# Kernel tuning notes

Hardware: AMD Instinct MI355X
Metric: run time of the kernel (lower is better)

The kernel has to match this reference:

```python
import jax, jax.numpy as jnp
import numpy as np

B, N, C = 128, 1024, 1
N_TIMES = 2
NUM_SUBSTEPS = 279  # trunc(dt_Output/dt_sub)+1 for default params


def setup_inputs() -> dict:
    key = jax.random.key(0)
    # small amplitude: d_to_u multiplies spectrum by k (up to N/2), keep CFL stable
    x = jax.random.normal(key, (B, N, C), dtype=jnp.float32) * 1e-3
    return {
        "x": x,
        "nu_para": jnp.float32(-3.0),
        "dt_Output_para": jnp.float32(-3.0),
        "cRatio_para": jnp.float32(0.1),
        "nTimes": N_TIMES,
        "num_substeps": NUM_SUBSTEPS,
    }


def _forward(x, nu_para, dt_Output_para, cRatio_para, nTimes, num_substeps):
    n = x.shape[1]
    L = 2.0 * np.pi
    k = (2.0 * np.pi / L) * jnp.arange(n // 2 + 1, dtype=jnp.float32)  # [n//2+1]
    ik = 1j * k

    # reparameterized physical params (sigmoid squashing, as in the torch module)
    nu = jax.nn.sigmoid(nu_para) * (0.5 - 0.01) + 0.01
    dt_out = jax.nn.sigmoid(dt_Output_para) * (0.1 - 0.001) + 0.001
    cR = jax.nn.sigmoid(cRatio_para) * (2.0 - 0.5) + 0.5

    d = jnp.transpose(x, (0, 2, 1))  # [B, C, N]
    # d_to_u: u = irfft(1j * rfft(d) * k)
    u = jnp.fft.irfft(1j * jnp.fft.rfft(d) * k, n=n)

    dt = dt_out / num_substeps
    # q = 1 - dt*cR*(k + nu*(1j*k)^2) ; (1j*k)^2 = -k^2 so q is real-valued
    q = 1.0 - dt * cR * (k - nu * k * k)

    def substep(u, _):
        uhat = jnp.fft.rfft(u)
        u2hat = jnp.fft.rfft(0.5 * u * u)
        u_new = jnp.fft.irfft((uhat - dt * ik * u2hat) / q, n=n)
        return u_new, None

    def outer(u, _):
        u, _ = jax.lax.scan(substep, u, None, length=num_substeps)
        return u, u

    _, usol = jax.lax.scan(outer, u, None, length=nTimes)  # [T, B, C, N]
    T = usol.shape[0]
    # torch.cat(usol, dim=1): [B, T*C, N] with time-major ordering
    usol = jnp.moveaxis(usol, 0, 1).reshape(usol.shape[1], T * usol.shape[2], n)

    # u_to_d: d_hat = -1j*rfft(u); d_hat[...,1:] /= k[1:]; d_hat[...,0] = 0
    d_hat = -1j * jnp.fft.rfft(usol)
    safe_k = jnp.where(k > 0, k, 1.0)
    d_hat = jnp.where(k > 0, d_hat / safe_k, jnp.zeros((), dtype=d_hat.dtype))
    dsol = jnp.fft.irfft(d_hat, n=n)  # [B, T*C, N]

    return jnp.transpose(dsol, (0, 2, 1))  # [B, N, T*C]


def reference(x, nu_para, dt_Output_para, cRatio_para, nTimes, num_substeps):
    return _forward(x, nu_para, dt_Output_para, cRatio_para, nTimes, num_substeps)
```

## Files before the change

### kernel.cpp

```cpp
#include <hip/hip_runtime.h>
#include <math.h>

#define NFFT 1024
#define BLK  512

template <int CTRL>
__device__ __forceinline__ float dppf(float v) {
    return __int_as_float(__builtin_amdgcn_update_dpp(
        0, __float_as_int(v), CTRL, 0xF, 0xF, true));
}
__device__ __forceinline__ float qx1(float v) { return dppf<0xB1>(v); }
__device__ __forceinline__ float qx2(float v) { return dppf<0x4E>(v); }
__device__ __forceinline__ float xr4(float v) { return dppf<0x1B>(dppf<0x141>(v)); }
__device__ __forceinline__ float xr8(float v) { return dppf<0x128>(v); }

__device__ __forceinline__ void pswap16(float v, float& lo, float& hi) {
    auto r = __builtin_amdgcn_permlane16_swap(__float_as_int(v), __float_as_int(v),
                                              false, false);
    lo = __int_as_float(r[0]);
    hi = __int_as_float(r[1]);
}
__device__ __forceinline__ void pswap32(float v, float& lo, float& hi) {
    auto r = __builtin_amdgcn_permlane32_swap(__float_as_int(v), __float_as_int(v),
                                              false, false);
    lo = __int_as_float(r[0]);
    hi = __int_as_float(r[1]);
}

#define DECL_G(G) float2 G##0, G##1, G##2, G##3, G##4, G##5, G##6, G##7,       \
                         G##8, G##9, G##10, G##11, G##12, G##13, G##14, G##15

#define GROW(Gd, d)                                                             \
    {   float sx = 0.0f, sy = 0.0f;                                             \
        _Pragma("unroll")                                                       \
        for (int ka = 0; ka < 16; ++ka) {                                       \
            const float ang = (float)((d) * ka) * 0.125f;                       \
            sx = fmaf(mv[ka], cospif(ang), sx);                                 \
            sy = fmaf(mv[ka], -sinpif(ang), sy);                                \
        }                                                                       \
        Gd = make_float2(sx, sy); }

#define BUILD_G(G)                                                              \
    GROW(G##0, 0)  GROW(G##1, 1)  GROW(G##2, 2)   GROW(G##3, 3)                 \
    GROW(G##4, 4)  GROW(G##5, 5)  GROW(G##6, 6)   GROW(G##7, 7)                 \
    GROW(G##8, 8)  GROW(G##9, 9)  GROW(G##10, 10) GROW(G##11, 11)               \
    GROW(G##12, 12) GROW(G##13, 13) GROW(G##14, 14) GROW(G##15, 15)

#define CTERM(G, j, A, B, C)                                                    \
    {   const float4 v = buf[par][(((w + (j)) & 7) << 6) + l];                  \
        ax0 = fmaf(G##A.x, v.x, ax0);  ax0 = fmaf(-G##A.y, v.y, ax0);           \
        ay0 = fmaf(G##A.x, v.y, ay0);  ay0 = fmaf( G##A.y, v.x, ay0);           \
        ax0 = fmaf(G##B.x, v.z, ax0);  ax0 = fmaf(-G##B.y, v.w, ax0);           \
        ay0 = fmaf(G##B.x, v.w, ay0);  ay0 = fmaf( G##B.y, v.z, ay0);           \
        ax1 = fmaf(G##C.x, v.x, ax1);  ax1 = fmaf(-G##C.y, v.y, ax1);           \
        ay1 = fmaf(G##C.x, v.y, ay1);  ay1 = fmaf( G##C.y, v.x, ay1);           \
        ax1 = fmaf(G##A.x, v.z, ax1);  ax1 = fmaf(-G##A.y, v.w, ax1);           \
        ay1 = fmaf(G##A.x, v.w, ay1);  ay1 = fmaf( G##A.y, v.z, ay1); }

#define EXCHANGE_G(G)                                                           \
    do {                                                                        \
        buf[par][tt] = make_float4(wt0.x * z0.x - wt0.y * z0.y,                 \
                                   wt0.x * z0.y + wt0.y * z0.x,                 \
                                   wt1.x * z1.x - wt1.y * z1.y,                 \
                                   wt1.x * z1.y + wt1.y * z1.x);                \
        __syncthreads();                                                        \
        float ax0 = 0.0f, ay0 = 0.0f, ax1 = 0.0f, ay1 = 0.0f;                   \
        CTERM(G, 0, 0, 1, 15)   CTERM(G, 1, 2, 3, 1)                            \
        CTERM(G, 2, 4, 5, 3)    CTERM(G, 3, 6, 7, 5)                            \
        CTERM(G, 4, 8, 9, 7)    CTERM(G, 5, 10, 11, 9)                          \
        CTERM(G, 6, 12, 13, 11) CTERM(G, 7, 14, 15, 13)                         \
        z0 = make_float2(cw0.x * ax0 - cw0.y * ay0, cw0.x * ay0 + cw0.y * ax0); \
        z1 = make_float2(cw1.x * ax1 - cw1.y * ay1, cw1.x * ay1 + cw1.y * ax1); \
        par ^= 1;                                                               \
    } while (0)

__global__ __launch_bounds__(BLK, 2)
void siva_kernel(const float* __restrict__ x,
                 const float* __restrict__ nu_p,
                 const float* __restrict__ dto_p,
                 const float* __restrict__ cr_p,
                 const int* __restrict__ nt_p,
                 const int* __restrict__ ns_p,
                 float* __restrict__ out) {
    __shared__ float4 buf[2][BLK];

    const int tt = threadIdx.x;
    const int b  = blockIdx.x;
    const int l  = tt & 63;
    const int w  = tt >> 6;
    const int a0 = 2 * w;
    const int a1 = 2 * w + 1;
    const int kb = (int)(__brev((unsigned)l) >> 26);

    const int nT   = nt_p[0];
    const int nsub = ns_p[0];

    const float nu  = (1.0f / (1.0f + expf(-nu_p[0])))  * (0.5f - 0.01f)  + 0.01f;
    const float dto = (1.0f / (1.0f + expf(-dto_p[0]))) * (0.1f - 0.001f) + 0.001f;
    const float cR  = (1.0f / (1.0f + expf(-cr_p[0])))  * (2.0f - 0.5f)   + 0.5f;
    const float dt   = dto / (float)nsub;
    const float dtcR = dt * cR;

    float2 wt0, wt1, cw0, cw1;
    {
        const float g0a = (float)(a0 * kb) * (1.0f / 512.0f);
        const float c0 = cospif(g0a), s0 = sinpif(g0a);
        wt0 = make_float2(c0, -s0);
        cw0 = make_float2(c0 * (1.0f / 1024.0f), s0 * (1.0f / 1024.0f));
        const float g1a = (float)(a1 * kb) * (1.0f / 512.0f);
        const float c1 = cospif(g1a), s1 = sinpif(g1a);
        wt1 = make_float2(c1, -s1);
        cw1 = make_float2(c1 * (1.0f / 1024.0f), s1 * (1.0f / 1024.0f));
    }

    float2 wf[6]; float sg[6]; float2 wi[6];
    #pragma unroll
    for (int s = 0; s < 6; ++s) {
        const int h = 32 >> s;
        const int lm = l & (h - 1);
        const bool hif = (l & h) != 0;
        const float a = (float)(lm * (32 / h)) * (1.0f / 32.0f);
        wf[s] = hif ? make_float2(cospif(a), -sinpif(a)) : make_float2(1.0f, 0.0f);
        sg[s] = hif ? -1.0f : 1.0f;
        const int h2 = 1 << s;
        const int lm2 = l & (h2 - 1);
        const float a2 = (float)lm2 / (float)h2;
        float2 wb = make_float2(cospif(a2), sinpif(a2));
        if ((l & h2) != 0) { wb.x = -wb.x; wb.y = -wb.y; }
        wi[s] = wb;
    }
    float2 cai[4], cbi[4];
    #pragma unroll
    for (int s = 0; s < 4; ++s) {
        const bool hif = (l & (1 << s)) != 0;
        cai[s] = hif ? wi[s] : make_float2(1.0f, 0.0f);
        cbi[s] = hif ? make_float2(1.0f, 0.0f) : wi[s];
    }

    auto fwd_s = [&](float2& zz, float bx, float by, int s) {
        const float tx = fmaf(sg[s], zz.x, bx);
        const float ty = fmaf(sg[s], zz.y, by);
        zz.x = tx * wf[s].x - ty * wf[s].y;
        zz.y = tx * wf[s].y + ty * wf[s].x;
    };
    auto inv_sf = [&](float2& zz, float px, float py, int s) {
        const float nx = fmaf(cai[s].x, zz.x, fmaf(-cai[s].y, zz.y,
                         fmaf(cbi[s].x, px, -cbi[s].y * py)));
        const float ny = fmaf(cai[s].x, zz.y, fmaf(cai[s].y, zz.x,
                         fmaf(cbi[s].x, py, cbi[s].y * px)));
        zz = make_float2(nx, ny);
    };
    auto fwd_one = [&](float2& zz, int s) {
        if (s == 0) {
            float lox, hix, loy, hiy;
            pswap32(zz.x, lox, hix); pswap32(zz.y, loy, hiy);
            const float tx = fmaf(sg[0], hix, lox);
            const float ty = fmaf(sg[0], hiy, loy);
            zz.x = tx * wf[0].x - ty * wf[0].y;
            zz.y = tx * wf[0].y + ty * wf[0].x;
        } else if (s == 1) {
            float lox, hix, loy, hiy;
            pswap16(zz.x, lox, hix); pswap16(zz.y, loy, hiy);
            const float tx = fmaf(sg[1], hix, lox);
            const float ty = fmaf(sg[1], hiy, loy);
            zz.x = tx * wf[1].x - ty * wf[1].y;
            zz.y = tx * wf[1].y + ty * wf[1].x;
        } else if (s == 2) fwd_s(zz, xr8(zz.x), xr8(zz.y), 2);
        else if (s == 3)   fwd_s(zz, xr4(zz.x), xr4(zz.y), 3);
        else if (s == 4)   fwd_s(zz, qx2(zz.x), qx2(zz.y), 4);
        else               fwd_s(zz, qx1(zz.x), qx1(zz.y), 5);
    };
    auto inv_one = [&](float2& zz, int s) {
        if (s == 0)      inv_sf(zz, qx1(zz.x), qx1(zz.y), 0);
        else if (s == 1) inv_sf(zz, qx2(zz.x), qx2(zz.y), 1);
        else if (s == 2) inv_sf(zz, xr4(zz.x), xr4(zz.y), 2);
        else if (s == 3) inv_sf(zz, xr8(zz.x), xr8(zz.y), 3);
        else if (s == 4) {
            float lox, hix, loy, hiy;
            pswap16(zz.x, lox, hix); pswap16(zz.y, loy, hiy);
            zz.x = fmaf(wi[4].x, hix, fmaf(-wi[4].y, hiy, lox));
            zz.y = fmaf(wi[4].x, hiy, fmaf( wi[4].y, hix, loy));
        } else {
            float lox, hix, loy, hiy;
            pswap32(zz.x, lox, hix); pswap32(zz.y, loy, hiy);
            zz.x = fmaf(wi[5].x, hix, fmaf(-wi[5].y, hiy, lox));
            zz.y = fmaf(wi[5].x, hiy, fmaf( wi[5].y, hix, loy));
        }
    };
    auto lane_fwd6 = [&](float2& za, float2& zb) {
        #pragma unroll
        for (int s = 0; s < 6; ++s) { fwd_one(za, s); fwd_one(zb, s); }
    };
    auto lane_inv6 = [&](float2& za, float2& zb) {
        #pragma unroll
        for (int s = 0; s < 6; ++s) { inv_one(za, s); inv_one(zb, s); }
    };

    DECL_G(gS);
    {
        float mv[16];
        #pragma unroll
        for (int ka = 0; ka < 16; ++ka) {
            const int k = kb + 64 * ka;
            const float kk = (k <= 512) ? (float)k : (float)(k - 1024);
            const float kab = fabsf(kk);
            const float q = 1.0f - dtcR * (kab - nu * kab * kab);
            const float kkS = (k == 0 || k == 512) ? 0.0f : kk;
            mv[ka] = (1.0f - dt * kkS) / q;
        }
        BUILD_G(gS)
    }

    int par = 0;
    float2 z0, z1;
    float u0, u1;

    z0 = make_float2(x[b * NFFT + 16 * l + a0], 0.0f);
    z1 = make_float2(x[b * NFFT + 16 * l + a1], 0.0f);
    {
        DECL_G(gD);
        {
            float mv[16];
            #pragma unroll
            for (int ka = 0; ka < 16; ++ka) {
                const int k = kb + 64 * ka;
                mv[ka] = (k <= 512) ? (float)k : (float)(k - 1024);
            }
            BUILD_G(gD)
        }
        lane_fwd6(z0, z1);
        EXCHANGE_G(gD);
        lane_inv6(z0, z1);
        u0 = -z0.y;
        u1 = -z1.y;
    }

    for (int ot = 0; ot < nT; ++ot) {
        for (int ss = 0; ss < nsub; ++ss) {
            z0 = make_float2(u0, 0.5f * u0 * u0);
            z1 = make_float2(u1, 0.5f * u1 * u1);
            lane_fwd6(z0, z1);
            EXCHANGE_G(gS);
            lane_inv6(z0, z1);
            u0 = z0.x;
            u1 = z1.x;
        }
        {
            DECL_G(gU);
            {
                float mv[16];
                #pragma unroll
                for (int ka = 0; ka < 16; ++ka) {
                    const int k = kb + 64 * ka;
                    const float kk = (k <= 512) ? (float)k : (float)(k - 1024);
                    mv[ka] = (k == 0) ? 0.0f : (1.0f / kk);
                }
                BUILD_G(gU)
            }
            z0 = make_float2(u0, 0.0f);
            z1 = make_float2(u1, 0.0f);
            lane_fwd6(z0, z1);
            EXCHANGE_G(gU);
            lane_inv6(z0, z1);
            out[(b * NFFT + 16 * l + a0) * nT + ot] = z0.y;
            out[(b * NFFT + 16 * l + a1) * nT + ot] = z1.y;
        }
    }
}

extern "C" void kernel_launch(void* const* d_in, const int* in_sizes, int n_in,
                              void* d_out, int out_size, void* d_ws, size_t ws_size,
                              hipStream_t stream) {
    const float* x     = (const float*)d_in[0];
    const float* nu_p  = (const float*)d_in[1];
    const float* dto_p = (const float*)d_in[2];
    const float* cr_p  = (const float*)d_in[3];
    const int*   nt_p  = (const int*)d_in[4];
    const int*   ns_p  = (const int*)d_in[5];
    float* out = (float*)d_out;

    const int B = in_sizes[0] / NFFT;
    siva_kernel<<<B, BLK, 0, stream>>>(x, nu_p, dto_p, cr_p, nt_p, ns_p, out);
}
```

Measured before the change: 713.3 us.

## Restructure FFT decomposition as 2x64x8 to halve cross-wave spectral multiply work

Changes the index decomposition of the 1024-point FFT so each thread's two points differ by 512. A radix-2 butterfly now runs in registers before the 64-lane stages, and the cross-wave stage becomes an 8-way mix instead of 16-way. The twiddle multiplies before and after the LDS exchange are folded into the last forward and first inverse lane stages, and the per-substep spectral operator matrices shrink from 16 to 8 complex entries per half. The aim is to cut the FMA count and register pressure in the 279-step inner loop, at the cost of more intricate twiddle bookkeeping that could introduce correctness bugs.

```diff
diff --git a/kernel.cpp b/kernel.cpp
--- a/kernel.cpp
+++ b/kernel.cpp
@@ -27,50 +27,38 @@
     hi = __int_as_float(r[1]);
 }
 
-#define DECL_G(G) float2 G##0, G##1, G##2, G##3, G##4, G##5, G##6, G##7,       \
-                         G##8, G##9, G##10, G##11, G##12, G##13, G##14, G##15
-
-#define GROW(Gd, d)                                                             \
+#define DECL_G8(G) float2 G##0, G##1, G##2, G##3, G##4, G##5, G##6, G##7
+
+#define GROW8(Gd, d)                                                            \
     {   float sx = 0.0f, sy = 0.0f;                                             \
         _Pragma("unroll")                                                       \
-        for (int ka = 0; ka < 16; ++ka) {                                       \
-            const float ang = (float)((d) * ka) * 0.125f;                       \
+        for (int ka = 0; ka < 8; ++ka) {                                        \
+            const float ang = (float)((d) * ka) * 0.25f;                        \
             sx = fmaf(mv[ka], cospif(ang), sx);                                 \
             sy = fmaf(mv[ka], -sinpif(ang), sy);                                \
         }                                                                       \
         Gd = make_float2(sx, sy); }
 
-#define BUILD_G(G)                                                              \
-    GROW(G##0, 0)  GROW(G##1, 1)  GROW(G##2, 2)   GROW(G##3, 3)                 \
-    GROW(G##4, 4)  GROW(G##5, 5)  GROW(G##6, 6)   GROW(G##7, 7)                 \
-    GROW(G##8, 8)  GROW(G##9, 9)  GROW(G##10, 10) GROW(G##11, 11)               \
-    GROW(G##12, 12) GROW(G##13, 13) GROW(G##14, 14) GROW(G##15, 15)
-
-#define CTERM(G, j, A, B, C)                                                    \
+#define BUILD_G8(G)                                                             \
+    GROW8(G##0, 0) GROW8(G##1, 1) GROW8(G##2, 2) GROW8(G##3, 3)                 \
+    GROW8(G##4, 4) GROW8(G##5, 5) GROW8(G##6, 6) GROW8(G##7, 7)
+
+#define CT8(GA, GB, j)                                                          \
     {   const float4 v = buf[par][(((w + (j)) & 7) << 6) + l];                  \
-        ax0 = fmaf(G##A.x, v.x, ax0);  ax0 = fmaf(-G##A.y, v.y, ax0);           \
-        ay0 = fmaf(G##A.x, v.y, ay0);  ay0 = fmaf( G##A.y, v.x, ay0);           \
-        ax0 = fmaf(G##B.x, v.z, ax0);  ax0 = fmaf(-G##B.y, v.w, ax0);           \
-        ay0 = fmaf(G##B.x, v.w, ay0);  ay0 = fmaf( G##B.y, v.z, ay0);           \
-        ax1 = fmaf(G##C.x, v.x, ax1);  ax1 = fmaf(-G##C.y, v.y, ax1);           \
-        ay1 = fmaf(G##C.x, v.y, ay1);  ay1 = fmaf( G##C.y, v.x, ay1);           \
-        ax1 = fmaf(G##A.x, v.z, ax1);  ax1 = fmaf(-G##A.y, v.w, ax1);           \
-        ay1 = fmaf(G##A.x, v.w, ay1);  ay1 = fmaf( G##A.y, v.z, ay1); }
-
-#define EXCHANGE_G(G)                                                           \
+        ax0 = fmaf(GA##j.x, v.x, ax0);  ax0 = fmaf(-GA##j.y, v.y, ax0);         \
+        ay0 = fmaf(GA##j.x, v.y, ay0);  ay0 = fmaf( GA##j.y, v.x, ay0);         \
+        ax1 = fmaf(GB##j.x, v.z, ax1);  ax1 = fmaf(-GB##j.y, v.w, ax1);         \
+        ay1 = fmaf(GB##j.x, v.w, ay1);  ay1 = fmaf( GB##j.y, v.z, ay1); }
+
+#define EXCHANGE8(GA, GB)                                                       \
     do {                                                                        \
-        buf[par][tt] = make_float4(wt0.x * z0.x - wt0.y * z0.y,                 \
-                                   wt0.x * z0.y + wt0.y * z0.x,                 \
-                                   wt1.x * z1.x - wt1.y * z1.y,                 \
-                                   wt1.x * z1.y + wt1.y * z1.x);                \
+        buf[par][tt] = make_float4(z0.x, z0.y, z1.x, z1.y);                     \
         __syncthreads();                                                        \
         float ax0 = 0.0f, ay0 = 0.0f, ax1 = 0.0f, ay1 = 0.0f;                   \
-        CTERM(G, 0, 0, 1, 15)   CTERM(G, 1, 2, 3, 1)                            \
-        CTERM(G, 2, 4, 5, 3)    CTERM(G, 3, 6, 7, 5)                            \
-        CTERM(G, 4, 8, 9, 7)    CTERM(G, 5, 10, 11, 9)                          \
-        CTERM(G, 6, 12, 13, 11) CTERM(G, 7, 14, 15, 13)                         \
-        z0 = make_float2(cw0.x * ax0 - cw0.y * ay0, cw0.x * ay0 + cw0.y * ax0); \
-        z1 = make_float2(cw1.x * ax1 - cw1.y * ay1, cw1.x * ay1 + cw1.y * ax1); \
+        CT8(GA, GB, 0) CT8(GA, GB, 1) CT8(GA, GB, 2) CT8(GA, GB, 3)             \
+        CT8(GA, GB, 4) CT8(GA, GB, 5) CT8(GA, GB, 6) CT8(GA, GB, 7)             \
+        z0 = make_float2(ax0, ay0);                                             \
+        z1 = make_float2(ax1, ay1);                                             \
         par ^= 1;                                                               \
     } while (0)
 
@@ -88,9 +76,9 @@
     const int b  = blockIdx.x;
     const int l  = tt & 63;
     const int w  = tt >> 6;
-    const int a0 = 2 * w;
-    const int a1 = 2 * w + 1;
-    const int kb = (int)(__brev((unsigned)l) >> 26);
+    const int R  = (int)(__brev((unsigned)l) >> 26);
+    const int kb0 = 2 * R;
+    const int kb1 = 2 * R + 1;
 
     const int nT   = nt_p[0];
     const int nsub = ns_p[0];
@@ -101,27 +89,44 @@
     const float dt   = dto / (float)nsub;
     const float dtcR = dt * cR;
 
-    float2 wt0, wt1, cw0, cw1;
+    float2 T128, cT128;
+    { const float a = (float)l * (1.0f / 64.0f);
+      const float c = cospif(a), s = sinpif(a);
+      T128  = make_float2(c, -s);
+      cT128 = make_float2(c,  s); }
+
+    float2 wtF0, wtF1;
+    float2 Cai0_0, Cai0_1, Cbi0_0, Cbi0_1;
     {
-        const float g0a = (float)(a0 * kb) * (1.0f / 512.0f);
-        const float c0 = cospif(g0a), s0 = sinpif(g0a);
-        wt0 = make_float2(c0, -s0);
-        cw0 = make_float2(c0 * (1.0f / 1024.0f), s0 * (1.0f / 1024.0f));
-        const float g1a = (float)(a1 * kb) * (1.0f / 512.0f);
-        const float c1 = cospif(g1a), s1 = sinpif(g1a);
-        wt1 = make_float2(c1, -s1);
-        cw1 = make_float2(c1 * (1.0f / 1024.0f), s1 * (1.0f / 1024.0f));
-    }
-
-    float2 wf[6]; float sg[6]; float2 wi[6];
+        const float sgn1 = (l & 1) ? -1.0f : 1.0f;
+        const float a0a = (float)(w * kb0) * (1.0f / 512.0f);
+        const float a1a = (float)(w * kb1) * (1.0f / 512.0f);
+        wtF0 = make_float2(cospif(a0a), -sinpif(a0a));
+        wtF1 = make_float2(cospif(a1a), -sinpif(a1a));
+        Cai0_0 = make_float2(sgn1 * cospif(a0a) * (1.0f / 1024.0f),
+                             sgn1 * sinpif(a0a) * (1.0f / 1024.0f));
+        Cai0_1 = make_float2(sgn1 * cospif(a1a) * (1.0f / 1024.0f),
+                             sgn1 * sinpif(a1a) * (1.0f / 1024.0f));
+        const int Rp = R ^ 32;
+        const float p0a = (float)(w * (2 * Rp)) * (1.0f / 512.0f);
+        const float p1a = (float)(w * (2 * Rp + 1)) * (1.0f / 512.0f);
+        Cbi0_0 = make_float2(cospif(p0a) * (1.0f / 1024.0f),
+                             sinpif(p0a) * (1.0f / 1024.0f));
+        Cbi0_1 = make_float2(cospif(p1a) * (1.0f / 1024.0f),
+                             sinpif(p1a) * (1.0f / 1024.0f));
+    }
+
+    float2 wf[5]; float sg[5]; float2 wi[6];
     #pragma unroll
     for (int s = 0; s < 6; ++s) {
         const int h = 32 >> s;
         const int lm = l & (h - 1);
         const bool hif = (l & h) != 0;
-        const float a = (float)(lm * (32 / h)) * (1.0f / 32.0f);
-        wf[s] = hif ? make_float2(cospif(a), -sinpif(a)) : make_float2(1.0f, 0.0f);
-        sg[s] = hif ? -1.0f : 1.0f;
+        if (s < 5) {
+            const float a = (float)(lm * (32 / h)) * (1.0f / 32.0f);
+            wf[s] = hif ? make_float2(cospif(a), -sinpif(a)) : make_float2(1.0f, 0.0f);
+            sg[s] = hif ? -1.0f : 1.0f;
+        }
         const int h2 = 1 << s;
         const int lm2 = l & (h2 - 1);
         const float a2 = (float)lm2 / (float)h2;
@@ -129,9 +134,10 @@
         if ((l & h2) != 0) { wb.x = -wb.x; wb.y = -wb.y; }
         wi[s] = wb;
     }
+    const float sg5 = (l & 1) ? -1.0f : 1.0f;
     float2 cai[4], cbi[4];
     #pragma unroll
-    for (int s = 0; s < 4; ++s) {
+    for (int s = 1; s < 4; ++s) {
         const bool hif = (l & (1 << s)) != 0;
         cai[s] = hif ? wi[s] : make_float2(1.0f, 0.0f);
         cbi[s] = hif ? make_float2(1.0f, 0.0f) : wi[s];
@@ -150,87 +156,158 @@
                          fmaf(cbi[s].x, py, cbi[s].y * px)));
         zz = make_float2(nx, ny);
     };
-    auto fwd_one = [&](float2& zz, int s) {
-        if (s == 0) {
+
+    auto fwd_all = [&](float2& z0, float2& z1) {
+        {
+            const float dxr = z0.x - z1.x, dyr = z0.y - z1.y;
+            z0 = make_float2(z0.x + z1.x, z0.y + z1.y);
+            z1 = make_float2(dxr * T128.x - dyr * T128.y,
+                             dxr * T128.y + dyr * T128.x);
+        }
+        {
             float lox, hix, loy, hiy;
-            pswap32(zz.x, lox, hix); pswap32(zz.y, loy, hiy);
-            const float tx = fmaf(sg[0], hix, lox);
-            const float ty = fmaf(sg[0], hiy, loy);
-            zz.x = tx * wf[0].x - ty * wf[0].y;
-            zz.y = tx * wf[0].y + ty * wf[0].x;
-        } else if (s == 1) {
+            pswap32(z0.x, lox, hix); pswap32(z0.y, loy, hiy);
+            float tx = fmaf(sg[0], hix, lox), ty = fmaf(sg[0], hiy, loy);
+            z0.x = tx * wf[0].x - ty * wf[0].y;
+            z0.y = tx * wf[0].y + ty * wf[0].x;
+            pswap32(z1.x, lox, hix); pswap32(z1.y, loy, hiy);
+            tx = fmaf(sg[0], hix, lox); ty = fmaf(sg[0], hiy, loy);
+            z1.x = tx * wf[0].x - ty * wf[0].y;
+            z1.y = tx * wf[0].y + ty * wf[0].x;
+        }
+        {
             float lox, hix, loy, hiy;
-            pswap16(zz.x, lox, hix); pswap16(zz.y, loy, hiy);
-            const float tx = fmaf(sg[1], hix, lox);
-            const float ty = fmaf(sg[1], hiy, loy);
-            zz.x = tx * wf[1].x - ty * wf[1].y;
-            zz.y = tx * wf[1].y + ty * wf[1].x;
-        } else if (s == 2) fwd_s(zz, xr8(zz.x), xr8(zz.y), 2);
-        else if (s == 3)   fwd_s(zz, xr4(zz.x), xr4(zz.y), 3);
-        else if (s == 4)   fwd_s(zz, qx2(zz.x), qx2(zz.y), 4);
-        else               fwd_s(zz, qx1(zz.x), qx1(zz.y), 5);
+            pswap16(z0.x, lox, hix); pswap16(z0.y, loy, hiy);
+            float tx = fmaf(sg[1], hix, lox), ty = fmaf(sg[1], hiy, loy);
+            z0.x = tx * wf[1].x - ty * wf[1].y;
+            z0.y = tx * wf[1].y + ty * wf[1].x;
+            pswap16(z1.x, lox, hix); pswap16(z1.y, loy, hiy);
+            tx = fmaf(sg[1], hix, lox); ty = fmaf(sg[1], hiy, loy);
+            z1.x = tx * wf[1].x - ty * wf[1].y;
+            z1.y = tx * wf[1].y + ty * wf[1].x;
+        }
+        fwd_s(z0, xr8(z0.x), xr8(z0.y), 2);  fwd_s(z1, xr8(z1.x), xr8(z1.y), 2);
+        fwd_s(z0, xr4(z0.x), xr4(z0.y), 3);  fwd_s(z1, xr4(z1.x), xr4(z1.y), 3);
+        fwd_s(z0, qx2(z0.x), qx2(z0.y), 4);  fwd_s(z1, qx2(z1.x), qx2(z1.y), 4);
+        {
+            const float px = qx1(z0.x), py = qx1(z0.y);
+            const float tx = fmaf(sg5, z0.x, px), ty = fmaf(sg5, z0.y, py);
+            z0.x = tx * wtF0.x - ty * wtF0.y;
+            z0.y = tx * wtF0.y + ty * wtF0.x;
+        }
+        {
+            const float px = qx1(z1.x), py = qx1(z1.y);
+            const float tx = fmaf(sg5, z1.x, px), ty = fmaf(sg5, z1.y, py);
+            z1.x = tx * wtF1.x - ty * wtF1.y;
+            z1.y = tx * wtF1.y + ty * wtF1.x;
+        }
     };
-    auto inv_one = [&](float2& zz, int s) {
-        if (s == 0)      inv_sf(zz, qx1(zz.x), qx1(zz.y), 0);
-        else if (s == 1) inv_sf(zz, qx2(zz.x), qx2(zz.y), 1);
-        else if (s == 2) inv_sf(zz, xr4(zz.x), xr4(zz.y), 2);
-        else if (s == 3) inv_sf(zz, xr8(zz.x), xr8(zz.y), 3);
-        else if (s == 4) {
+
+    auto inv_all = [&](float2& z0, float2& z1) {
+        {
+            const float px = qx1(z0.x), py = qx1(z0.y);
+            const float nx = fmaf(Cai0_0.x, z0.x, fmaf(-Cai0_0.y, z0.y,
+                             fmaf(Cbi0_0.x, px, -Cbi0_0.y * py)));
+            const float ny = fmaf(Cai0_0.x, z0.y, fmaf(Cai0_0.y, z0.x,
+                             fmaf(Cbi0_0.x, py, Cbi0_0.y * px)));
+            z0 = make_float2(nx, ny);
+        }
+        {
+            const float px = qx1(z1.x), py = qx1(z1.y);
+            const float nx = fmaf(Cai0_1.x, z1.x, fmaf(-Cai0_1.y, z1.y,
+                             fmaf(Cbi0_1.x, px, -Cbi0_1.y * py)));
+            const float ny = fmaf(Cai0_1.x, z1.y, fmaf(Cai0_1.y, z1.x,
+                             fmaf(Cbi0_1.x, py, Cbi0_1.y * px)));
+            z1 = make_float2(nx, ny);
+        }
+        inv_sf(z0, qx2(z0.x), qx2(z0.y), 1);  inv_sf(z1, qx2(z1.x), qx2(z1.y), 1);
+        inv_sf(z0, xr4(z0.x), xr4(z0.y), 2);  inv_sf(z1, xr4(z1.x), xr4(z1.y), 2);
+        inv_sf(z0, xr8(z0.x), xr8(z0.y), 3);  inv_sf(z1, xr8(z1.x), xr8(z1.y), 3);
+        {
             float lox, hix, loy, hiy;
-            pswap16(zz.x, lox, hix); pswap16(zz.y, loy, hiy);
-            zz.x = fmaf(wi[4].x, hix, fmaf(-wi[4].y, hiy, lox));
-            zz.y = fmaf(wi[4].x, hiy, fmaf( wi[4].y, hix, loy));
-        } else {
+            pswap16(z0.x, lox, hix); pswap16(z0.y, loy, hiy);
+            z0.x = fmaf(wi[4].x, hix, fmaf(-wi[4].y, hiy, lox));
+            z0.y = fmaf(wi[4].x, hiy, fmaf( wi[4].y, hix, loy));
+            pswap16(z1.x, lox, hix); pswap16(z1.y, loy, hiy);
+            z1.x = fmaf(wi[4].x, hix, fmaf(-wi[4].y, hiy, lox));
+            z1.y = fmaf(wi[4].x, hiy, fmaf( wi[4].y, hix, loy));
+        }
+        {
             float lox, hix, loy, hiy;
-            pswap32(zz.x, lox, hix); pswap32(zz.y, loy, hiy);
-            zz.x = fmaf(wi[5].x, hix, fmaf(-wi[5].y, hiy, lox));
-            zz.y = fmaf(wi[5].x, hiy, fmaf( wi[5].y, hix, loy));
+            pswap32(z0.x, lox, hix); pswap32(z0.y, loy, hiy);
+            z0.x = fmaf(wi[5].x, hix, fmaf(-wi[5].y, hiy, lox));
+            z0.y = fmaf(wi[5].x, hiy, fmaf( wi[5].y, hix, loy));
+            pswap32(z1.x, lox, hix); pswap32(z1.y, loy, hiy);
+            z1.x = fmaf(wi[5].x, hix, fmaf(-wi[5].y, hiy, lox));
+            z1.y = fmaf(wi[5].x, hiy, fmaf( wi[5].y, hix, loy));
+        }
+        {
+            const float tx = z1.x * cT128.x - z1.y * cT128.y;
+            const float ty = z1.x * cT128.y + z1.y * cT128.x;
+            z1 = make_float2(z0.x - tx, z0.y - ty);
+            z0 = make_float2(z0.x + tx, z0.y + ty);
         }
     };
-    auto lane_fwd6 = [&](float2& za, float2& zb) {
+
+    DECL_G8(gS0); DECL_G8(gS1);
+    {
+        float mv[8];
         #pragma unroll
-        for (int s = 0; s < 6; ++s) { fwd_one(za, s); fwd_one(zb, s); }
-    };
-    auto lane_inv6 = [&](float2& za, float2& zb) {
-        #pragma unroll
-        for (int s = 0; s < 6; ++s) { inv_one(za, s); inv_one(zb, s); }
-    };
-
-    DECL_G(gS);
-    {
-        float mv[16];
-        #pragma unroll
-        for (int ka = 0; ka < 16; ++ka) {
-            const int k = kb + 64 * ka;
+        for (int ka = 0; ka < 8; ++ka) {
+            const int k = kb0 + 128 * ka;
             const float kk = (k <= 512) ? (float)k : (float)(k - 1024);
             const float kab = fabsf(kk);
             const float q = 1.0f - dtcR * (kab - nu * kab * kab);
             const float kkS = (k == 0 || k == 512) ? 0.0f : kk;
             mv[ka] = (1.0f - dt * kkS) / q;
         }
-        BUILD_G(gS)
+        BUILD_G8(gS0)
+    }
+    {
+        float mv[8];
+        #pragma unroll
+        for (int ka = 0; ka < 8; ++ka) {
+            const int k = kb1 + 128 * ka;
+            const float kk = (k <= 512) ? (float)k : (float)(k - 1024);
+            const float kab = fabsf(kk);
+            const float q = 1.0f - dtcR * (kab - nu * kab * kab);
+            const float kkS = (k == 0 || k == 512) ? 0.0f : kk;
+            mv[ka] = (1.0f - dt * kkS) / q;
+        }
+        BUILD_G8(gS1)
     }
 
     int par = 0;
     float2 z0, z1;
     float u0, u1;
-
-    z0 = make_float2(x[b * NFFT + 16 * l + a0], 0.0f);
-    z1 = make_float2(x[b * NFFT + 16 * l + a1], 0.0f);
+    const int n0 = 8 * l + w;
+    const int n1 = 512 + 8 * l + w;
+
+    z0 = make_float2(x[b * NFFT + n0], 0.0f);
+    z1 = make_float2(x[b * NFFT + n1], 0.0f);
     {
-        DECL_G(gD);
-        {
-            float mv[16];
+        DECL_G8(gD0); DECL_G8(gD1);
+        {
+            float mv[8];
             #pragma unroll
-            for (int ka = 0; ka < 16; ++ka) {
-                const int k = kb + 64 * ka;
+            for (int ka = 0; ka < 8; ++ka) {
+                const int k = kb0 + 128 * ka;
                 mv[ka] = (k <= 512) ? (float)k : (float)(k - 1024);
             }
-            BUILD_G(gD)
-        }
-        lane_fwd6(z0, z1);
-        EXCHANGE_G(gD);
-        lane_inv6(z0, z1);
+            BUILD_G8(gD0)
+        }
+        {
+            float mv[8];
+            #pragma unroll
+            for (int ka = 0; ka < 8; ++ka) {
+                const int k = kb1 + 128 * ka;
+                mv[ka] = (k <= 512) ? (float)k : (float)(k - 1024);
+            }
+            BUILD_G8(gD1)
+        }
+        fwd_all(z0, z1);
+        EXCHANGE8(gD0, gD1);
+        inv_all(z0, z1);
         u0 = -z0.y;
         u1 = -z1.y;
     }
@@ -239,31 +316,41 @@
         for (int ss = 0; ss < nsub; ++ss) {
             z0 = make_float2(u0, 0.5f * u0 * u0);
             z1 = make_float2(u1, 0.5f * u1 * u1);
-            lane_fwd6(z0, z1);
-            EXCHANGE_G(gS);
-            lane_inv6(z0, z1);
+            fwd_all(z0, z1);
+            EXCHANGE8(gS0, gS1);
+            inv_all(z0, z1);
             u0 = z0.x;
             u1 = z1.x;
         }
         {
-            DECL_G(gU);
+            DECL_G8(gU0); DECL_G8(gU1);
             {
-                float mv[16];
+                float mv[8];
                 #pragma unroll
-                for (int ka = 0; ka < 16; ++ka) {
-                    const int k = kb + 64 * ka;
+                for (int ka = 0; ka < 8; ++ka) {
+                    const int k = kb0 + 128 * ka;
                     const float kk = (k <= 512) ? (float)k : (float)(k - 1024);
                     mv[ka] = (k == 0) ? 0.0f : (1.0f / kk);
                 }
-                BUILD_G(gU)
+                BUILD_G8(gU0)
+            }
+            {
+                float mv[8];
+                #pragma unroll
+                for (int ka = 0; ka < 8; ++ka) {
+                    const int k = kb1 + 128 * ka;
+                    const float kk = (k <= 512) ? (float)k : (float)(k - 1024);
+                    mv[ka] = (k == 0) ? 0.0f : (1.0f / kk);
+                }
+                BUILD_G8(gU1)
             }
             z0 = make_float2(u0, 0.0f);
             z1 = make_float2(u1, 0.0f);
-            lane_fwd6(z0, z1);
-            EXCHANGE_G(gU);
-            lane_inv6(z0, z1);
-            out[(b * NFFT + 16 * l + a0) * nT + ot] = z0.y;
-            out[(b * NFFT + 16 * l + a1) * nT + ot] = z1.y;
+            fwd_all(z0, z1);
+            EXCHANGE8(gU0, gU1);
+            inv_all(z0, z1);
+            out[(b * NFFT + n0) * nT + ot] = z0.y;
+            out[(b * NFFT + n1) * nT + ot] = z1.y;
         }
     }
 }
```

Measured after the change: 665.5 us. -6.7%, faster.
